# Performance work log

Measured on AMD Instinct MI355X. Metric: run time of the kernel, lower is better.

## Reference

```python
import jax, jax.numpy as jnp
import numpy as np

PAD = 0  # padding token id; its embedding row is zero (padding_idx)


def setup_inputs() -> dict:
    key = jax.random.key(0)
    k1, k2, k3 = jax.random.split(key, 3)
    HOPS, VOCAB, D = 3, 50257, 128
    B, M, S = 32, 512, 6        # batch, memory slots, tokens per slot
    T, L = 128, 64              # trees per example, tokens per (flattened) tree
    # hop+1 embedding tables, normal(0, 0.1) like the torch init
    C = 0.1 * jax.random.normal(k1, (HOPS + 1, VOCAB, D), dtype=jnp.float32)
    C = C.at[:, PAD].set(0.0)   # padding_idx row = 0
    story = jax.random.randint(k2, (B, M, S), 0, VOCAB, dtype=jnp.int32)
    kb_tokens = jax.random.randint(k3, (B, T, L), 0, VOCAB, dtype=jnp.int32)
    return {"C": C, "story": story, "kb_tokens": kb_tokens}


def reference(C, story, kb_tokens):
    # C: [hops+1, V, D]; story: [B, M, S]; kb_tokens: [B, T, L]
    hops = C.shape[0] - 1
    B = story.shape[0]
    D = C.shape[-1]
    u = jnp.zeros((B, D), dtype=C.dtype)
    for hop in range(hops):
        # key memory: story slots (sum over tokens) + tree memories (sum over
        # all subtree tokens == dfs recursive sum, since PAD embeds to zero)
        m_story_A = jnp.take(C[hop], story, axis=0).sum(axis=2)       # [B,M,D]
        tree_A = jnp.take(C[hop], kb_tokens, axis=0).sum(axis=2)      # [B,T,D]
        m_A = jnp.concatenate([m_story_A, tree_A], axis=1)            # [B,M+T,D]
        prob = jax.nn.softmax(jnp.einsum("bmd,bd->bm", m_A, u), axis=1)
        # value memory with next-hop table
        m_story_C = jnp.take(C[hop + 1], story, axis=0).sum(axis=2)
        tree_C = jnp.take(C[hop + 1], kb_tokens, axis=0).sum(axis=2)
        m_C = jnp.concatenate([m_story_C, tree_C], axis=1)
        o_k = jnp.einsum("bm,bmd->bd", prob, m_C)
        u = u + o_k
    return u
```

## Files before the change

### kernel.cpp

```cpp
#include <hip/hip_runtime.h>
#include <math.h>

constexpr int HOPS  = 3;
constexpr int VOCAB = 50257;
constexpr int DIM   = 128;
constexpr int NB    = 32;
constexpr int NM    = 512;
constexpr int NS    = 6;
constexpr int NT    = 128;
constexpr int NL    = 64;
constexpr int SLOTS = NM + NT;
constexpr size_t TS = (size_t)VOCAB * DIM;
constexpr size_t TABSTRIDE = (size_t)NB * SLOTS * DIM;
constexpr int CHUNKS = SLOTS / 64;
constexpr int TREE_BLOCKS  = NB * NT / 4;
constexpr int STORY_BLOCKS = NB * NM / 4;


__device__ __forceinline__ void addf4(float4& a, const float4& v) {
    a.x += v.x; a.y += v.y; a.z += v.z; a.w += v.w;
}
__device__ __forceinline__ void halfred(float4& a) {
    a.x += __shfl_xor(a.x, 32); a.y += __shfl_xor(a.y, 32);
    a.z += __shfl_xor(a.z, 32); a.w += __shfl_xor(a.w, 32);
}

__global__ __launch_bounds__(256) void gather_fused(
    const float* __restrict__ C, const int* __restrict__ story,
    const int* __restrict__ kb, float* __restrict__ msum)
{
    const int wave = threadIdx.x >> 6, lane = threadIdx.x & 63;
    const int half = lane >> 5, q = lane & 31;
    const float* Cb = C + TS + (size_t)q * 4;
    float4 a0 = {0,0,0,0}, a1 = {0,0,0,0}, a2 = {0,0,0,0};

    if (blockIdx.x < TREE_BLOCKS) {
        const int g = blockIdx.x * 4 + wave;
        const int tok = kb[(size_t)g * NL + lane];
        #pragma unroll 8
        for (int i = 0; i < NL / 2; ++i) {
            int s = __shfl(tok, 2 * i + half);
            const float* p = Cb + (size_t)s * DIM;
            addf4(a0, *(const float4*)(p));
            addf4(a1, *(const float4*)(p + TS));
            addf4(a2, *(const float4*)(p + 2 * TS));
        }
        halfred(a0); halfred(a1); halfred(a2);
        if (half == 0) {
            const int b = g >> 7, tr = g & (NT - 1);
            const size_t o = ((size_t)b * SLOTS + NM + tr) * DIM + q * 4;
            *(float4*)(msum + o)                 = a0;
            *(float4*)(msum + o + TABSTRIDE)     = a1;
            *(float4*)(msum + o + 2 * TABSTRIDE) = a2;
        }
    } else {
        const int g = (blockIdx.x - TREE_BLOCKS) * 4 + wave;
        const int* idx = story + (size_t)g * NS;
        int tok = (lane < NS) ? idx[lane] : 0;
        #pragma unroll
        for (int i = 0; i < NS / 2; ++i) {
            int s = __shfl(tok, 2 * i + half);
            const float* p = Cb + (size_t)s * DIM;
            addf4(a0, *(const float4*)(p));
            addf4(a1, *(const float4*)(p + TS));
            addf4(a2, *(const float4*)(p + 2 * TS));
        }
        halfred(a0); halfred(a1); halfred(a2);
        if (half == 0) {
            const int b = g >> 9, slot = g & (NM - 1);
            const size_t o = ((size_t)b * SLOTS + slot) * DIM + q * 4;
            *(float4*)(msum + o)                 = a0;
            *(float4*)(msum + o + TABSTRIDE)     = a1;
            *(float4*)(msum + o + 2 * TABSTRIDE) = a2;
        }
    }
}

__global__ __launch_bounds__(256) void hop0_k(
    const float* __restrict__ msum, float* __restrict__ u)
{
    const int b = blockIdx.x, t = threadIdx.x, d = t & (DIM - 1), sub = t >> 7;
    const float* mC = msum + ((size_t)b * SLOTS + sub * (SLOTS / 2)) * DIM + d;
    float acc = 0.f;
    #pragma unroll 16
    for (int m = 0; m < SLOTS / 2; ++m) acc += mC[(size_t)m * DIM];
    __shared__ float red[256];
    red[t] = acc;
    __syncthreads();
    if (t < DIM) u[b * DIM + t] = (red[t] + red[t + 128]) * (1.f / SLOTS);
}

__device__ __forceinline__ float dot128(const float* __restrict__ row,
                                        const float* __restrict__ u_s)
{
    float4 acc = {0.f, 0.f, 0.f, 0.f};
    #pragma unroll
    for (int i = 0; i < DIM / 4; ++i) {
        float4 r  = ((const float4*)row)[i];
        float4 uu = ((const float4*)u_s)[i];
        acc.x = fmaf(r.x, uu.x, acc.x);
        acc.y = fmaf(r.y, uu.y, acc.y);
        acc.z = fmaf(r.z, uu.z, acc.z);
        acc.w = fmaf(r.w, uu.w, acc.w);
    }
    return (acc.x + acc.y) + (acc.z + acc.w);
}

__global__ __launch_bounds__(256) void scores_softmax_k(
    const float* __restrict__ msum, const float* __restrict__ u,
    float* __restrict__ sc, int tab)
{
    const int b = blockIdx.x, t = threadIdx.x, wv = t >> 6, ln = t & 63;
    __shared__ float u_s[DIM];
    __shared__ float red[4];
    if (t < DIM) u_s[t] = u[b * DIM + t];
    __syncthreads();

    const float* mA = msum + (size_t)tab * TABSTRIDE + (size_t)b * SLOTS * DIM;
    float s0 = dot128(mA + (size_t)t * DIM, u_s);
    float s1 = dot128(mA + (size_t)(t + 256) * DIM, u_s);
    float s2 = (t < SLOTS - 512) ? dot128(mA + (size_t)(t + 512) * DIM, u_s)
                                 : -INFINITY;

    float lmax = fmaxf(fmaxf(s0, s1), s2);
    #pragma unroll
    for (int off = 32; off > 0; off >>= 1) lmax = fmaxf(lmax, __shfl_xor(lmax, off));
    if (ln == 0) red[wv] = lmax;
    __syncthreads();
    lmax = fmaxf(fmaxf(red[0], red[1]), fmaxf(red[2], red[3]));
    __syncthreads();

    float e0 = expf(s0 - lmax), e1 = expf(s1 - lmax);
    float e2 = (t < SLOTS - 512) ? expf(s2 - lmax) : 0.f;
    float lsum = e0 + e1 + e2;
    #pragma unroll
    for (int off = 32; off > 0; off >>= 1) lsum += __shfl_xor(lsum, off);
    if (ln == 0) red[wv] = lsum;
    __syncthreads();
    const float inv = 1.0f / (red[0] + red[1] + red[2] + red[3]);

    float* s = sc + b * SLOTS;
    s[t] = e0 * inv;
    s[t + 256] = e1 * inv;
    if (t < SLOTS - 512) s[t + 512] = e2 * inv;
}

__global__ __launch_bounds__(256) void weighted_k(
    const float* __restrict__ msum, const float* __restrict__ probs,
    float* __restrict__ u, int tab)
{
    const int b = blockIdx.x / CHUNKS, chunk = blockIdx.x % CHUNKS;
    const int t = threadIdx.x, d = t & (DIM - 1), sub = t >> 7;
    __shared__ float p[64];
    if (t < 64) p[t] = probs[b * SLOTS + chunk * 64 + t];
    __syncthreads();
    const float* mC = msum + (size_t)tab * TABSTRIDE +
                      ((size_t)b * SLOTS + chunk * 64 + sub * 32) * DIM + d;
    float acc = 0.f;
    #pragma unroll
    for (int m = 0; m < 32; ++m) acc = fmaf(p[sub * 32 + m], mC[(size_t)m * DIM], acc);
    __shared__ float red[256];
    red[t] = acc;
    __syncthreads();
    if (t < DIM) atomicAdd(&u[b * DIM + d], red[t] + red[t + 128]);
}

extern "C" void kernel_launch(void* const* d_in, const int* in_sizes, int n_in,
                              void* d_out, int out_size, void* d_ws, size_t ws_size,
                              hipStream_t stream) {
    const float* C     = (const float*)d_in[0];
    const int*   story = (const int*)d_in[1];
    const int*   kb    = (const int*)d_in[2];
    float*       u     = (float*)d_out;
    float*       msum  = (float*)d_ws;
    float*       sc    = msum + 3 * TABSTRIDE;

    gather_fused<<<TREE_BLOCKS + STORY_BLOCKS, 256, 0, stream>>>(C, story, kb, msum);
    hop0_k<<<NB, 256, 0, stream>>>(msum , u);

    for (int hop = 1; hop < HOPS; ++hop) {
        scores_softmax_k<<<NB, 256, 0, stream>>>(msum, u, sc, hop - 1);
        weighted_k<<<NB * CHUNKS, 256, 0, stream>>>(msum, sc, u, hop);
    }
}
```

Measured before the change: 240.1 us.

## Convert embedding tables to interleaved fp16 and gather/store memories in half

Adds a pre-pass that converts tables 1..3 to fp16, interleaved per vocab row so the three tables' rows are contiguous. The gather then reads half8 vectors with 16 lanes per slot and 16 slots per block, and stores the slot sums in fp16, which also halves the traffic in the later hop kernels. The conversion pass reads the full 3x50257x128 fp32 tables every call, roughly 77MB, which likely costs more than the gathers it saves. fp16 storage also reduces accuracy.

```diff
diff --git a/kernel.cpp b/kernel.cpp
--- a/kernel.cpp
+++ b/kernel.cpp
@@ -13,101 +13,137 @@
 constexpr size_t TS = (size_t)VOCAB * DIM;
 constexpr size_t TABSTRIDE = (size_t)NB * SLOTS * DIM;
 constexpr int CHUNKS = SLOTS / 64;
-constexpr int TREE_BLOCKS  = NB * NT / 4;
-constexpr int STORY_BLOCKS = NB * NM / 4;
-
-
-__device__ __forceinline__ void addf4(float4& a, const float4& v) {
-    a.x += v.x; a.y += v.y; a.z += v.z; a.w += v.w;
-}
-__device__ __forceinline__ void halfred(float4& a) {
-    a.x += __shfl_xor(a.x, 32); a.y += __shfl_xor(a.y, 32);
-    a.z += __shfl_xor(a.z, 32); a.w += __shfl_xor(a.w, 32);
+
+constexpr size_t CH_ELEMS = (size_t)VOCAB * 3 * DIM;
+constexpr int NE8 = (int)(CH_ELEMS / 8);
+
+typedef _Float16 half8 __attribute__((ext_vector_type(8)));
+
+constexpr int TREE_BLOCKS  = NB * NT / 16;
+constexpr int STORY_BLOCKS = NB * NM / 16;
+constexpr int GATHER_BLOCKS = TREE_BLOCKS + STORY_BLOCKS;
+
+__global__ __launch_bounds__(256) void convert_k(
+    const float* __restrict__ C, _Float16* __restrict__ Ch)
+{
+    const int e8 = blockIdx.x * 256 + threadIdx.x;
+    if (e8 >= NE8) return;
+    const size_t base = (size_t)e8 * 8;
+    const size_t v    = base / 384;
+    const int    rem  = (int)(base % 384);
+    const int    tab  = rem >> 7;
+    const int    d    = rem & 127;
+    const float* src = C + (size_t)(1 + tab) * TS + v * DIM + d;
+    float4 f0 = *(const float4*)(src);
+    float4 f1 = *(const float4*)(src + 4);
+    half8 h;
+    h[0] = (_Float16)f0.x; h[1] = (_Float16)f0.y;
+    h[2] = (_Float16)f0.z; h[3] = (_Float16)f0.w;
+    h[4] = (_Float16)f1.x; h[5] = (_Float16)f1.y;
+    h[6] = (_Float16)f1.z; h[7] = (_Float16)f1.w;
+    *(half8*)(Ch + base) = h;
 }
 
 __global__ __launch_bounds__(256) void gather_fused(
-    const float* __restrict__ C, const int* __restrict__ story,
-    const int* __restrict__ kb, float* __restrict__ msum)
+    const _Float16* __restrict__ Ch, const int* __restrict__ story,
+    const int* __restrict__ kb, _Float16* __restrict__ msum)
 {
     const int wave = threadIdx.x >> 6, lane = threadIdx.x & 63;
-    const int half = lane >> 5, q = lane & 31;
-    const float* Cb = C + TS + (size_t)q * 4;
-    float4 a0 = {0,0,0,0}, a1 = {0,0,0,0}, a2 = {0,0,0,0};
-
-    if (blockIdx.x < TREE_BLOCKS) {
-        const int g = blockIdx.x * 4 + wave;
-        const int tok = kb[(size_t)g * NL + lane];
-        #pragma unroll 8
-        for (int i = 0; i < NL / 2; ++i) {
-            int s = __shfl(tok, 2 * i + half);
-            const float* p = Cb + (size_t)s * DIM;
-            addf4(a0, *(const float4*)(p));
-            addf4(a1, *(const float4*)(p + TS));
-            addf4(a2, *(const float4*)(p + 2 * TS));
-        }
-        halfred(a0); halfred(a1); halfred(a2);
-        if (half == 0) {
-            const int b = g >> 7, tr = g & (NT - 1);
-            const size_t o = ((size_t)b * SLOTS + NM + tr) * DIM + q * 4;
-            *(float4*)(msum + o)                 = a0;
-            *(float4*)(msum + o + TABSTRIDE)     = a1;
-            *(float4*)(msum + o + 2 * TABSTRIDE) = a2;
+    const int q = lane >> 4, l16 = lane & 15;
+    const int qbase = lane & 48;
+
+    float a0[8] = {0,0,0,0,0,0,0,0};
+    float a1[8] = {0,0,0,0,0,0,0,0};
+    float a2[8] = {0,0,0,0,0,0,0,0};
+
+    const bool is_tree = (blockIdx.x % 5) == 0;
+    int b, slot;
+
+    if (is_tree) {
+        const int g = (blockIdx.x / 5) * 16 + wave * 4 + q;
+        b = g >> 7; slot = NM + (g & (NT - 1));
+        const int* idx = kb + (size_t)g * NL;
+        #pragma unroll
+        for (int o = 0; o < 4; ++o) {
+            const int tokv = idx[o * 16 + l16];
+            #pragma unroll
+            for (int i = 0; i < 16; ++i) {
+                const int s = __shfl(tokv, qbase + i);
+                const _Float16* p = Ch + (size_t)s * (3 * DIM) + l16 * 8;
+                half8 v0 = *(const half8*)(p);
+                half8 v1 = *(const half8*)(p + DIM);
+                half8 v2 = *(const half8*)(p + 2 * DIM);
+                #pragma unroll
+                for (int j = 0; j < 8; ++j) {
+                    a0[j] += (float)v0[j];
+                    a1[j] += (float)v1[j];
+                    a2[j] += (float)v2[j];
+                }
+            }
         }
     } else {
-        const int g = (blockIdx.x - TREE_BLOCKS) * 4 + wave;
+        const int sb = blockIdx.x - blockIdx.x / 5 - 1;
+        const int g = sb * 16 + wave * 4 + q;
+        b = g >> 9; slot = g & (NM - 1);
         const int* idx = story + (size_t)g * NS;
-        int tok = (lane < NS) ? idx[lane] : 0;
+        const int tokv = (l16 < NS) ? idx[l16] : 0;
         #pragma unroll
-        for (int i = 0; i < NS / 2; ++i) {
-            int s = __shfl(tok, 2 * i + half);
-            const float* p = Cb + (size_t)s * DIM;
-            addf4(a0, *(const float4*)(p));
-            addf4(a1, *(const float4*)(p + TS));
-            addf4(a2, *(const float4*)(p + 2 * TS));
+        for (int i = 0; i < NS; ++i) {
+            const int s = __shfl(tokv, qbase + i);
+            const _Float16* p = Ch + (size_t)s * (3 * DIM) + l16 * 8;
+            half8 v0 = *(const half8*)(p);
+            half8 v1 = *(const half8*)(p + DIM);
+            half8 v2 = *(const half8*)(p + 2 * DIM);
+            #pragma unroll
+            for (int j = 0; j < 8; ++j) {
+                a0[j] += (float)v0[j];
+                a1[j] += (float)v1[j];
+                a2[j] += (float)v2[j];
+            }
         }
-        halfred(a0); halfred(a1); halfred(a2);
-        if (half == 0) {
-            const int b = g >> 9, slot = g & (NM - 1);
-            const size_t o = ((size_t)b * SLOTS + slot) * DIM + q * 4;
-            *(float4*)(msum + o)                 = a0;
-            *(float4*)(msum + o + TABSTRIDE)     = a1;
-            *(float4*)(msum + o + 2 * TABSTRIDE) = a2;
-        }
-    }
+    }
+
+    const size_t o = ((size_t)b * SLOTS + slot) * DIM + l16 * 8;
+    half8 h0, h1, h2;
+    #pragma unroll
+    for (int j = 0; j < 8; ++j) {
+        h0[j] = (_Float16)a0[j]; h1[j] = (_Float16)a1[j]; h2[j] = (_Float16)a2[j];
+    }
+    *(half8*)(msum + o)                 = h0;
+    *(half8*)(msum + o + TABSTRIDE)     = h1;
+    *(half8*)(msum + o + 2 * TABSTRIDE) = h2;
 }
 
 __global__ __launch_bounds__(256) void hop0_k(
-    const float* __restrict__ msum, float* __restrict__ u)
+    const _Float16* __restrict__ msum, float* __restrict__ u)
 {
     const int b = blockIdx.x, t = threadIdx.x, d = t & (DIM - 1), sub = t >> 7;
-    const float* mC = msum + ((size_t)b * SLOTS + sub * (SLOTS / 2)) * DIM + d;
+    const _Float16* mC = msum + ((size_t)b * SLOTS + sub * (SLOTS / 2)) * DIM + d;
     float acc = 0.f;
     #pragma unroll 16
-    for (int m = 0; m < SLOTS / 2; ++m) acc += mC[(size_t)m * DIM];
+    for (int m = 0; m < SLOTS / 2; ++m) acc += (float)mC[(size_t)m * DIM];
     __shared__ float red[256];
     red[t] = acc;
     __syncthreads();
     if (t < DIM) u[b * DIM + t] = (red[t] + red[t + 128]) * (1.f / SLOTS);
 }
 
-__device__ __forceinline__ float dot128(const float* __restrict__ row,
-                                        const float* __restrict__ u_s)
-{
-    float4 acc = {0.f, 0.f, 0.f, 0.f};
-    #pragma unroll
-    for (int i = 0; i < DIM / 4; ++i) {
-        float4 r  = ((const float4*)row)[i];
-        float4 uu = ((const float4*)u_s)[i];
-        acc.x = fmaf(r.x, uu.x, acc.x);
-        acc.y = fmaf(r.y, uu.y, acc.y);
-        acc.z = fmaf(r.z, uu.z, acc.z);
-        acc.w = fmaf(r.w, uu.w, acc.w);
-    }
-    return (acc.x + acc.y) + (acc.z + acc.w);
+__device__ __forceinline__ float dot128h(const _Float16* __restrict__ row,
+                                         const float* __restrict__ u_s)
+{
+    float acc = 0.f;
+    const half8* r8 = (const half8*)row;
+    #pragma unroll
+    for (int i = 0; i < DIM / 8; ++i) {
+        half8 h = r8[i];
+        #pragma unroll
+        for (int j = 0; j < 8; ++j) acc = fmaf((float)h[j], u_s[8 * i + j], acc);
+    }
+    return acc;
 }
 
 __global__ __launch_bounds__(256) void scores_softmax_k(
-    const float* __restrict__ msum, const float* __restrict__ u,
+    const _Float16* __restrict__ msum, const float* __restrict__ u,
     float* __restrict__ sc, int tab)
 {
     const int b = blockIdx.x, t = threadIdx.x, wv = t >> 6, ln = t & 63;
@@ -116,10 +152,10 @@
     if (t < DIM) u_s[t] = u[b * DIM + t];
     __syncthreads();
 
-    const float* mA = msum + (size_t)tab * TABSTRIDE + (size_t)b * SLOTS * DIM;
-    float s0 = dot128(mA + (size_t)t * DIM, u_s);
-    float s1 = dot128(mA + (size_t)(t + 256) * DIM, u_s);
-    float s2 = (t < SLOTS - 512) ? dot128(mA + (size_t)(t + 512) * DIM, u_s)
+    const _Float16* mA = msum + (size_t)tab * TABSTRIDE + (size_t)b * SLOTS * DIM;
+    float s0 = dot128h(mA + (size_t)t * DIM, u_s);
+    float s1 = dot128h(mA + (size_t)(t + 256) * DIM, u_s);
+    float s2 = (t < SLOTS - 512) ? dot128h(mA + (size_t)(t + 512) * DIM, u_s)
                                  : -INFINITY;
 
     float lmax = fmaxf(fmaxf(s0, s1), s2);
@@ -146,7 +182,7 @@
 }
 
 __global__ __launch_bounds__(256) void weighted_k(
-    const float* __restrict__ msum, const float* __restrict__ probs,
+    const _Float16* __restrict__ msum, const float* __restrict__ probs,
     float* __restrict__ u, int tab)
 {
     const int b = blockIdx.x / CHUNKS, chunk = blockIdx.x % CHUNKS;
@@ -154,11 +190,12 @@
     __shared__ float p[64];
     if (t < 64) p[t] = probs[b * SLOTS + chunk * 64 + t];
     __syncthreads();
-    const float* mC = msum + (size_t)tab * TABSTRIDE +
-                      ((size_t)b * SLOTS + chunk * 64 + sub * 32) * DIM + d;
+    const _Float16* mC = msum + (size_t)tab * TABSTRIDE +
+                         ((size_t)b * SLOTS + chunk * 64 + sub * 32) * DIM + d;
     float acc = 0.f;
     #pragma unroll
-    for (int m = 0; m < 32; ++m) acc = fmaf(p[sub * 32 + m], mC[(size_t)m * DIM], acc);
+    for (int m = 0; m < 32; ++m)
+        acc = fmaf(p[sub * 32 + m], (float)mC[(size_t)m * DIM], acc);
     __shared__ float red[256];
     red[t] = acc;
     __syncthreads();
@@ -172,10 +209,13 @@
     const int*   story = (const int*)d_in[1];
     const int*   kb    = (const int*)d_in[2];
     float*       u     = (float*)d_out;
-    float*       msum  = (float*)d_ws;
-    float*       sc    = msum + 3 * TABSTRIDE;
-
-    gather_fused<<<TREE_BLOCKS + STORY_BLOCKS, 256, 0, stream>>>(C, story, kb, msum);
+
+    _Float16* Ch   = (_Float16*)d_ws;
+    _Float16* msum = Ch + CH_ELEMS;
+    float*    sc   = (float*)(msum + 3 * TABSTRIDE);
+
+    convert_k<<<(NE8 + 255) / 256, 256, 0, stream>>>(C, Ch);
+    gather_fused<<<GATHER_BLOCKS, 256, 0, stream>>>(Ch, story, kb, msum);
     hop0_k<<<NB, 256, 0, stream>>>(msum , u);
 
     for (int hop = 1; hop < HOPS; ++hop) {
```

Measured after the change: 221.1 us. 7.9% less time.
